# Kernel optimization log

Hardware: AMD Instinct MI355X
Metric: run time of the kernel (lower is better)

Reference implementation:

```python
import jax, jax.numpy as jnp
import numpy as np

# Math note: feat = cat([ctx_i, asp_j, ctx_i*asp_j]) dotted with w_u [6H,1]
# decomposes as ctx_i.w1 + asp_j.w2 + (ctx_i*asp_j).w3 where w_u = cat([w1,w2,w3]).
# This lets us compute the full [B, L1, L2] alignment matrix with three small
# contractions instead of L1*L2 concat+matmul launches, with identical math.

def setup_inputs() -> dict:
    key = jax.random.key(0)
    k1, k2, k3 = jax.random.split(key, 3)
    B, L1, L2, D = 64, 512, 32, 600  # D = 2*hidden_dim
    ctx = jax.random.normal(k1, (B, L1, D), dtype=jnp.float32)
    asp = jax.random.normal(k2, (B, L2, D), dtype=jnp.float32)
    w_u = jax.random.normal(k3, (3 * D, 1), dtype=jnp.float32)
    return {"batch_size": B, "ctx": ctx, "asp": asp, "w_u": w_u}

def reference(batch_size, ctx, asp, w_u):
    D = ctx.shape[-1]
    w = w_u[:, 0]
    w1, w2, w3 = w[:D], w[D:2 * D], w[2 * D:]
    ctx_term = ctx @ w1                                  # [B, L1]
    asp_term = asp @ w2                                  # [B, L2]
    cross = jnp.einsum('bid,bjd->bij', ctx * w3, asp)    # [B, L1, L2]
    return ctx_term[:, :, None] + asp_term[:, None, :] + cross
```

## Files before the change

### kernel.cpp

```cpp
#include <hip/hip_runtime.h>
#include <hip/hip_bf16.h>

typedef float  f32x4  __attribute__((ext_vector_type(4)));
typedef short  bf16x8 __attribute__((ext_vector_type(8)));
typedef short  s16x4  __attribute__((ext_vector_type(4)));

#define NB   64
#define NL1  512
#define NL2  32
#define ND   600
#define NDP  640
#define NW1  608
#define ROWS 64

static __device__ __forceinline__ short f2bf(float f) {
    __hip_bfloat16 h = __float2bfloat16(f);
    return __builtin_bit_cast(short, h);
}

__global__ __launch_bounds__(256, 2)
void align_kernel(const float* __restrict__ ctx,
                  const float* __restrict__ asp,
                  const float* __restrict__ wu,
                  float* __restrict__ out)
{
    __shared__ short aspw3[NL2 * NDP];
    __shared__ float w1s[NW1];
    __shared__ float ctterm[ROWS];
    __shared__ float aspterm[NL2];

    const int tid     = threadIdx.x;
    const int lane    = tid & 63;
    const int wid     = tid >> 6;
    const int b       = blockIdx.x;
    const int rowbase = blockIdx.y * ROWS;

    const int r16 = lane & 15;
    const int g   = lane >> 4;
    const int jx  = lane & 7;
    const float* actx = ctx + ((size_t)b * NL1 + rowbase + wid * 16 + r16) * ND + 8 * g;

    float4 v0 = *(const float4*)(actx);
    float4 v1 = *(const float4*)(actx + 4);

    for (int i = tid; i < NW1; i += 256)
        w1s[i] = (i < ND) ? wu[i] : 0.f;

    {
        const int j   = tid >> 3;
        const int e   = tid & 7;
        const int jxs = j & 7;

        aspw3[j * NDP + ((75 ^ jxs) << 3) + e] = 0;

        const int sub = tid & 7;
        const float* arow = asp + ((size_t)b * NL2 + j) * ND;
        float at = 0.f;
        #pragma unroll
        for (int m = 0; m < 19; ++m) {
            const int k = m * 32 + sub * 4;
            if (k < ND) {
                const float4 v  = *(const float4*)(arow + k);
                const float4 w2 = *(const float4*)(wu + ND + k);
                const float4 w3 = *(const float4*)(wu + 2 * ND + k);
                at += v.x * w2.x + v.y * w2.y + v.z * w2.z + v.w * w2.w;
                s16x4 h;
                h.x = f2bf(v.x * w3.x);
                h.y = f2bf(v.y * w3.y);
                h.z = f2bf(v.z * w3.z);
                h.w = f2bf(v.w * w3.w);
                const int c = (k >> 3) ^ jxs;
                *(s16x4*)&aspw3[j * NDP + (c << 3) + (k & 7)] = h;
            }
        }
        at += __shfl_xor(at, 1);
        at += __shfl_xor(at, 2);
        at += __shfl_xor(at, 4);
        if (sub == 0) aspterm[j] = at;
    }
    __syncthreads();

    f32x4 acc0 = {0.f, 0.f, 0.f, 0.f};
    f32x4 acc1 = {0.f, 0.f, 0.f, 0.f};
    float ct = 0.f;

    #pragma unroll 1
    for (int s = 0; s < 19; ++s) {
        float4 n0 = make_float4(0.f, 0.f, 0.f, 0.f);
        float4 n1 = make_float4(0.f, 0.f, 0.f, 0.f);
        if (s < 17) {
            n0 = *(const float4*)(actx + (s + 1) * 32);
            n1 = *(const float4*)(actx + (s + 1) * 32 + 4);
        } else if (s == 17) {
            if (g < 3) {
                n0 = *(const float4*)(actx + 18 * 32);
                n1 = *(const float4*)(actx + 18 * 32 + 4);
            }
        }

        const int k0 = s * 32;
        const float4 w1a = *(const float4*)&w1s[k0 + 8 * g];
        const float4 w1b = *(const float4*)&w1s[k0 + 8 * g + 4];
        ct += v0.x * w1a.x + v0.y * w1a.y + v0.z * w1a.z + v0.w * w1a.w
            + v1.x * w1b.x + v1.y * w1b.y + v1.z * w1b.z + v1.w * w1b.w;
        bf16x8 af;
        af[0] = f2bf(v0.x); af[1] = f2bf(v0.y); af[2] = f2bf(v0.z); af[3] = f2bf(v0.w);
        af[4] = f2bf(v1.x); af[5] = f2bf(v1.y); af[6] = f2bf(v1.z); af[7] = f2bf(v1.w);
        const int c = ((s * 4 + g) ^ jx) << 3;
        const bf16x8 b0 = *(const bf16x8*)&aspw3[r16 * NDP + c];
        const bf16x8 b1 = *(const bf16x8*)&aspw3[(16 + r16) * NDP + c];
        acc0 = __builtin_amdgcn_mfma_f32_16x16x32_bf16(af, b0, acc0, 0, 0, 0);
        acc1 = __builtin_amdgcn_mfma_f32_16x16x32_bf16(af, b1, acc1, 0, 0, 0);

        v0 = n0; v1 = n1;
    }

    ct += __shfl_xor(ct, 16);
    ct += __shfl_xor(ct, 32);
    if (lane < 16) ctterm[wid * 16 + lane] = ct;
    __syncthreads();

    const float atj0 = aspterm[r16];
    const float atj1 = aspterm[16 + r16];
    float* orow = out + ((size_t)b * NL1 + rowbase + wid * 16 + g * 4) * NL2;
    #pragma unroll
    for (int r = 0; r < 4; ++r) {
        const float cterm = ctterm[wid * 16 + g * 4 + r];
        orow[r * NL2 + r16]      = acc0[r] + cterm + atj0;
        orow[r * NL2 + 16 + r16] = acc1[r] + cterm + atj1;
    }
}

extern "C" void kernel_launch(void* const* d_in, const int* in_sizes, int n_in,
                              void* d_out, int out_size, void* d_ws, size_t ws_size,
                              hipStream_t stream) {
    (void)in_sizes; (void)n_in; (void)d_ws; (void)ws_size; (void)out_size;
    const float* ctx = (const float*)d_in[1];
    const float* asp = (const float*)d_in[2];
    const float* wu  = (const float*)d_in[3];
    float* out = (float*)d_out;
    dim3 grid(NB, NL1 / ROWS);
    align_kernel<<<grid, 256, 0, stream>>>(ctx, asp, wu, out);
}
```

Baseline: 21.92 us.

## Compute ctx·w1 term via extra MFMA and deepen ctx prefetch

Replaces the per-lane fp32 dot product for the ctx·w1 term, its cross-lane shuffle reduction and its shared-memory write plus barrier with a third bf16 MFMA against a broadcast w1 vector held in shared memory. It also prefetches ctx two iterations ahead instead of one to hide global-load latency. This trades fp32 accuracy on the ctx_term for bf16 and raises register pressure from the extra accumulator and prefetch registers.

```diff
diff --git a/kernel.cpp b/kernel.cpp
--- a/kernel.cpp
+++ b/kernel.cpp
@@ -25,8 +25,7 @@
                   float* __restrict__ out)
 {
     __shared__ short aspw3[NL2 * NDP];
-    __shared__ float w1s[NW1];
-    __shared__ float ctterm[ROWS];
+    __shared__ short w1bf[NW1];
     __shared__ float aspterm[NL2];
 
     const int tid     = threadIdx.x;
@@ -42,9 +41,11 @@
 
     float4 v0 = *(const float4*)(actx);
     float4 v1 = *(const float4*)(actx + 4);
+    float4 n0 = *(const float4*)(actx + 32);
+    float4 n1 = *(const float4*)(actx + 36);
 
     for (int i = tid; i < NW1; i += 256)
-        w1s[i] = (i < ND) ? wu[i] : 0.f;
+        w1bf[i] = (i < ND) ? f2bf(wu[i]) : (short)0;
 
     {
         const int j   = tid >> 3;
@@ -82,50 +83,44 @@
 
     f32x4 acc0 = {0.f, 0.f, 0.f, 0.f};
     f32x4 acc1 = {0.f, 0.f, 0.f, 0.f};
-    float ct = 0.f;
+    f32x4 acc2 = {0.f, 0.f, 0.f, 0.f};
 
     #pragma unroll 1
     for (int s = 0; s < 19; ++s) {
-        float4 n0 = make_float4(0.f, 0.f, 0.f, 0.f);
-        float4 n1 = make_float4(0.f, 0.f, 0.f, 0.f);
-        if (s < 17) {
-            n0 = *(const float4*)(actx + (s + 1) * 32);
-            n1 = *(const float4*)(actx + (s + 1) * 32 + 4);
-        } else if (s == 17) {
+        float4 p0 = make_float4(0.f, 0.f, 0.f, 0.f);
+        float4 p1 = make_float4(0.f, 0.f, 0.f, 0.f);
+        if (s < 16) {
+            p0 = *(const float4*)(actx + (s + 2) * 32);
+            p1 = *(const float4*)(actx + (s + 2) * 32 + 4);
+        } else if (s == 16) {
             if (g < 3) {
-                n0 = *(const float4*)(actx + 18 * 32);
-                n1 = *(const float4*)(actx + 18 * 32 + 4);
+                p0 = *(const float4*)(actx + 18 * 32);
+                p1 = *(const float4*)(actx + 18 * 32 + 4);
             }
         }
 
         const int k0 = s * 32;
-        const float4 w1a = *(const float4*)&w1s[k0 + 8 * g];
-        const float4 w1b = *(const float4*)&w1s[k0 + 8 * g + 4];
-        ct += v0.x * w1a.x + v0.y * w1a.y + v0.z * w1a.z + v0.w * w1a.w
-            + v1.x * w1b.x + v1.y * w1b.y + v1.z * w1b.z + v1.w * w1b.w;
         bf16x8 af;
         af[0] = f2bf(v0.x); af[1] = f2bf(v0.y); af[2] = f2bf(v0.z); af[3] = f2bf(v0.w);
         af[4] = f2bf(v1.x); af[5] = f2bf(v1.y); af[6] = f2bf(v1.z); af[7] = f2bf(v1.w);
         const int c = ((s * 4 + g) ^ jx) << 3;
         const bf16x8 b0 = *(const bf16x8*)&aspw3[r16 * NDP + c];
         const bf16x8 b1 = *(const bf16x8*)&aspw3[(16 + r16) * NDP + c];
+        const bf16x8 wf = *(const bf16x8*)&w1bf[k0 + 8 * g];
         acc0 = __builtin_amdgcn_mfma_f32_16x16x32_bf16(af, b0, acc0, 0, 0, 0);
         acc1 = __builtin_amdgcn_mfma_f32_16x16x32_bf16(af, b1, acc1, 0, 0, 0);
+        acc2 = __builtin_amdgcn_mfma_f32_16x16x32_bf16(af, wf, acc2, 0, 0, 0);
 
         v0 = n0; v1 = n1;
+        n0 = p0; n1 = p1;
     }
-
-    ct += __shfl_xor(ct, 16);
-    ct += __shfl_xor(ct, 32);
-    if (lane < 16) ctterm[wid * 16 + lane] = ct;
-    __syncthreads();
 
     const float atj0 = aspterm[r16];
     const float atj1 = aspterm[16 + r16];
     float* orow = out + ((size_t)b * NL1 + rowbase + wid * 16 + g * 4) * NL2;
     #pragma unroll
     for (int r = 0; r < 4; ++r) {
-        const float cterm = ctterm[wid * 16 + g * 4 + r];
+        const float cterm = acc2[r];
         orow[r * NL2 + r16]      = acc0[r] + cterm + atj0;
         orow[r * NL2 + 16 + r16] = acc1[r] + cterm + atj1;
     }
```

New measurement: 21.84 us. No clear change (-0.4%).
